# Performance work log

Measured on AMD Instinct MI355X. Metric: run time of the kernel, lower is better.

Reference implementation:

```python
import jax, jax.numpy as jnp
import numpy as np

VOCAB, INPUT, HIDDEN = 50000, 512, 1024
BATCH, MAX_LEN = 64, 256


def setup_inputs() -> dict:
    key = jax.random.key(0)
    ks = jax.random.split(key, 16)
    s = 0.02
    return {
        "last_output": jax.random.randint(ks[0], (BATCH,), 0, VOCAB),
        "last_hidden": jax.random.normal(ks[1], (BATCH, HIDDEN), jnp.float32),
        "encoder_outputs": jax.random.normal(ks[2], (MAX_LEN, BATCH, HIDDEN), jnp.float32),
        # embedding table (padding_idx=0 just means row 0 is a pad row; math is a plain gather)
        "embedding": jax.random.uniform(ks[3], (VOCAB, INPUT), jnp.float32, -0.25, 0.25),
        # concat attention: Linear(2H -> H) and v [H]
        "attn_W": jax.random.normal(ks[4], (HIDDEN, 2 * HIDDEN), jnp.float32) * s,
        "attn_b": jnp.zeros((HIDDEN,), jnp.float32),
        "v": jax.random.normal(ks[5], (HIDDEN,), jnp.float32) * s,
        # GRU (single layer): input size = INPUT + HIDDEN, gate order r,z,n (torch order)
        "W_ih": jax.random.normal(ks[6], (3 * HIDDEN, INPUT + HIDDEN), jnp.float32) * s,
        "W_hh": jax.random.uniform(ks[7], (3 * HIDDEN, HIDDEN), jnp.float32, -0.01, 0.01),
        "b_ih": jnp.zeros((3 * HIDDEN,), jnp.float32),
        "b_hh": jnp.zeros((3 * HIDDEN,), jnp.float32),
        # output projection Linear(2H -> vocab)
        "out_W": jax.random.normal(ks[8], (VOCAB, 2 * HIDDEN), jnp.float32) * s,
        "out_b": jnp.zeros((VOCAB,), jnp.float32),
    }


def reference(last_output, last_hidden, encoder_outputs, embedding,
              attn_W, attn_b, v, W_ih, W_hh, b_ih, b_hh, out_W, out_b):
    T, B, H = encoder_outputs.shape
    # --- embedding lookup: [B, INPUT]
    emb = embedding[last_output]

    # --- concat (Bahdanau-style, no tanh in original) attention, vectorized over T
    hid = jnp.broadcast_to(last_hidden[None], (T, B, H))
    cat = jnp.concatenate([hid, encoder_outputs], axis=-1)          # [T,B,2H]
    energy = jnp.einsum('tbk,hk->tbh', cat, attn_W) + attn_b        # [T,B,H]
    scores = jnp.einsum('tbh,h->bt', energy, v)                     # [B,T]
    attn = jax.nn.softmax(scores, axis=1)                           # [B,T]

    # --- context: [B,H]
    context = jnp.einsum('bt,tbh->bh', attn, encoder_outputs)

    # --- single GRU step (torch gate order r,z,n)
    x = jnp.concatenate([emb, context], axis=-1)                    # [B, INPUT+H]
    gi = x @ W_ih.T + b_ih                                          # [B,3H]
    gh = last_hidden @ W_hh.T + b_hh                                # [B,3H]
    i_r, i_z, i_n = jnp.split(gi, 3, axis=-1)
    h_r, h_z, h_n = jnp.split(gh, 3, axis=-1)
    r = jax.nn.sigmoid(i_r + h_r)
    z = jax.nn.sigmoid(i_z + h_z)
    n = jnp.tanh(i_n + r * h_n)
    h_new = (1.0 - z) * n + z * last_hidden                         # [B,H]

    # --- output projection + log_softmax over vocab
    logits = jnp.concatenate([h_new, context], axis=-1) @ out_W.T + out_b
    logp = jax.nn.log_softmax(logits, axis=-1)                      # [B,VOCAB]
    return logp, h_new
```

## Files before the change

kernel.cpp:

```cpp
#include <hip/hip_runtime.h>
#include <cstddef>

#define VOCAB  50000
#define INPUT  512
#define HIDDEN 1024
#define BATCH  64
#define MAXLEN 256
#define NBLK   625

typedef float  f32x4 __attribute__((ext_vector_type(4)));
typedef __bf16 bf16x8 __attribute__((ext_vector_type(8)));

__device__ __forceinline__ bf16x8 cvt8(float4 a, float4 b) {
    bf16x8 r;
    r[0] = (__bf16)a.x; r[1] = (__bf16)a.y; r[2] = (__bf16)a.z; r[3] = (__bf16)a.w;
    r[4] = (__bf16)b.x; r[5] = (__bf16)b.y; r[6] = (__bf16)b.z; r[7] = (__bf16)b.w;
    return r;
}

__global__ void k_u2_part(const float* __restrict__ attn_W, const float* __restrict__ v,
                          float* __restrict__ u2p) {
    int bid = blockIdx.x, tid = threadIdx.x;
    int hq = bid >> 4, kc = bid & 15;
    int kl = tid & 63, hg = tid >> 6;
    int k = kc * 64 + kl;
    float acc = 0.f;
    int h0 = hq * 256 + hg * 64;
#pragma unroll 8
    for (int h = h0; h < h0 + 64; ++h)
        acc += v[h] * attn_W[(size_t)h * (2 * HIDDEN) + HIDDEN + k];
    __shared__ float red[4][64];
    red[hg][kl] = acc;
    __syncthreads();
    if (tid < 64)
        u2p[hq * 1024 + kc * 64 + tid] =
            red[0][tid] + red[1][tid] + red[2][tid] + red[3][tid];
}

__global__ __launch_bounds__(256) void k_att(const float* __restrict__ enc,
                                             const float* __restrict__ u2p,
                                             float* __restrict__ mpart,
                                             float* __restrict__ lpart,
                                             float* __restrict__ ctxp) {
    int bid = blockIdx.x, tid = threadIdx.x;
    int b = bid >> 2, tq = bid & 3, t0 = tq * 64;
    __shared__ float u2s[1024];
    __shared__ float s_lds[64];
    __shared__ float p_lds[64];
    for (int i = tid; i < 1024; i += 256)
        u2s[i] = u2p[i] + u2p[1024 + i] + u2p[2048 + i] + u2p[3072 + i];
    __syncthreads();
    int w = tid >> 6, lane = tid & 63;
#pragma unroll 2
    for (int it = 0; it < 16; ++it) {
        int t = t0 + w * 16 + it;
        const float* row = enc + ((size_t)t * BATCH + b) * HIDDEN;
        float acc = 0.f;
#pragma unroll
        for (int i = 0; i < 4; ++i) {
            float4 e = *(const float4*)(row + lane * 4 + i * 256);
            float4 u = *(const float4*)(&u2s[lane * 4 + i * 256]);
            acc += e.x * u.x + e.y * u.y + e.z * u.z + e.w * u.w;
        }
#pragma unroll
        for (int off = 32; off; off >>= 1) acc += __shfl_down(acc, off, 64);
        if (lane == 0) s_lds[w * 16 + it] = acc;
    }
    __syncthreads();
    float m = -INFINITY;
#pragma unroll 8
    for (int t = 0; t < 64; ++t) m = fmaxf(m, s_lds[t]);
    if (tid < 64) p_lds[tid] = expf(s_lds[tid] - m);
    __syncthreads();
    float l = 0.f;
#pragma unroll 8
    for (int t = 0; t < 64; ++t) l += p_lds[t];
    float4 acc = {0.f, 0.f, 0.f, 0.f};
    const float* ebase = enc + ((size_t)t0 * BATCH + b) * HIDDEN + tid * 4;
#pragma unroll 4
    for (int t = 0; t < 64; ++t) {
        float p = p_lds[t];
        float4 e = *(const float4*)(ebase + (size_t)t * (BATCH * HIDDEN));
        acc.x += p * e.x; acc.y += p * e.y; acc.z += p * e.z; acc.w += p * e.w;
    }
    int o = b * 4 + tq;
    *(float4*)(ctxp + (size_t)o * 1024 + tid * 4) = acc;
    if (tid == 0) { mpart[o] = m; lpart[o] = l; }
}

__global__ void k_att_comb(const float* __restrict__ mpart, const float* __restrict__ lpart,
                           const float* __restrict__ ctxp,
                           const int* __restrict__ last_output,
                           const float* __restrict__ embedding,
                           const float* __restrict__ hid,
                           __bf16* __restrict__ x_bf, __bf16* __restrict__ hid_bf,
                           __bf16* __restrict__ y_bf) {
    int b = blockIdx.x >> 2, hc = blockIdx.x & 3, tid = threadIdx.x;
    float m0 = mpart[b * 4 + 0], m1 = mpart[b * 4 + 1];
    float m2 = mpart[b * 4 + 2], m3 = mpart[b * 4 + 3];
    float M = fmaxf(fmaxf(m0, m1), fmaxf(m2, m3));
    float w0 = expf(m0 - M), w1 = expf(m1 - M), w2 = expf(m2 - M), w3 = expf(m3 - M);
    float denom = lpart[b * 4 + 0] * w0 + lpart[b * 4 + 1] * w1 +
                  lpart[b * 4 + 2] * w2 + lpart[b * 4 + 3] * w3;
    float inv = 1.f / denom;
    int h = hc * 256 + tid;
    const float* cp = ctxp + (size_t)b * 4096 + h;
    float c = (w0 * cp[0] + w1 * cp[1024] + w2 * cp[2048] + w3 * cp[3072]) * inv;
    x_bf[b * 1536 + INPUT + h]  = (__bf16)c;
    y_bf[b * 2048 + HIDDEN + h] = (__bf16)c;
    if (hc < 2)
        x_bf[b * 1536 + hc * 256 + tid] =
            (__bf16)embedding[(size_t)last_output[b] * INPUT + hc * 256 + tid];
    hid_bf[b * HIDDEN + hc * 256 + tid] = (__bf16)hid[b * HIDDEN + hc * 256 + tid];
}

__device__ __forceinline__ void gemm_tile(const float* __restrict__ W,
                                          const float* __restrict__ bias,
                                          const __bf16* __restrict__ A,
                                          float* __restrict__ out,
                                          int N, int K, int jt, int tid) {
    int wid = tid >> 6, lane = tid & 63;
    int j  = jt * 16 + (lane & 15);
    int kg = (lane >> 4) * 8;
    int kchunk = K >> 2;
    int kbeg = wid * kchunk, kend = kbeg + kchunk;
    const float*  wrow = W + (size_t)j * K;
    const __bf16* arow = A + (size_t)(lane & 15) * K;
    f32x4 acc[4] = {};
    for (int k0 = kbeg; k0 < kend; k0 += 32) {
        int kk = k0 + kg;
        float4 w0 = *(const float4*)(wrow + kk);
        float4 w1 = *(const float4*)(wrow + kk + 4);
        bf16x8 bw = cvt8(w0, w1);
#pragma unroll
        for (int mt = 0; mt < 4; ++mt) {
            bf16x8 av = *(const bf16x8*)(arow + (size_t)mt * 16 * K + kk);
            acc[mt] = __builtin_amdgcn_mfma_f32_16x16x32_bf16(av, bw, acc[mt], 0, 0, 0);
        }
    }
    __shared__ float lds[4][1024];
#pragma unroll
    for (int mt = 0; mt < 4; ++mt)
#pragma unroll
        for (int r = 0; r < 4; ++r) {
            int m = mt * 16 + (lane >> 4) * 4 + r;
            lds[wid][m * 16 + (lane & 15)] = acc[mt][r];
        }
    __syncthreads();
#pragma unroll
    for (int o = tid; o < 1024; o += 256) {
        float s = lds[0][o] + lds[1][o] + lds[2][o] + lds[3][o];
        int m = o >> 4, jl = o & 15;
        out[(size_t)m * N + jt * 16 + jl] = s + bias[jt * 16 + jl];
    }
}

__global__ __launch_bounds__(256) void k_gemm_gru(const float* __restrict__ W_ih,
                                                  const float* __restrict__ b_ih,
                                                  const __bf16* __restrict__ x_bf,
                                                  float* __restrict__ Gi,
                                                  const float* __restrict__ W_hh,
                                                  const float* __restrict__ b_hh,
                                                  const __bf16* __restrict__ hid_bf,
                                                  float* __restrict__ Gh) {
    int bid = blockIdx.x, tid = threadIdx.x;
    if (bid < 192) gemm_tile(W_ih, b_ih, x_bf,  Gi, 3072, 1536, bid,       tid);
    else           gemm_tile(W_hh, b_hh, hid_bf, Gh, 3072, 1024, bid - 192, tid);
}

__global__ void k_combine(const float* __restrict__ Gi, const float* __restrict__ Gh,
                          const float* __restrict__ hid, float* __restrict__ hnew_out,
                          __bf16* __restrict__ y_bf) {
    int idx = blockIdx.x * 256 + threadIdx.x;
    int b = idx >> 10, h = idx & 1023;
    const float* gi = Gi + (size_t)b * 3072;
    const float* gh = Gh + (size_t)b * 3072;
    float r  = 1.f / (1.f + expf(-(gi[h] + gh[h])));
    float z  = 1.f / (1.f + expf(-(gi[1024 + h] + gh[1024 + h])));
    float n  = tanhf(gi[2048 + h] + r * gh[2048 + h]);
    float hp = hid[b * HIDDEN + h];
    float hn = (1.f - z) * n + z * hp;
    hnew_out[b * HIDDEN + h] = hn;
    y_bf[b * 2048 + h] = (__bf16)hn;
}

__global__ __launch_bounds__(256) void k_gemv(const float* __restrict__ W,
                                              const float* __restrict__ bias,
                                              const __bf16* __restrict__ A,
                                              float* __restrict__ out,
                                              float* __restrict__ mw,
                                              float* __restrict__ sw) {
    int bid = blockIdx.x, tid = threadIdx.x;
    int wid = tid >> 6, lane = tid & 63;
    int kg = (lane >> 4) * 8;
    int kbeg = wid * 512;
    int j0 = bid * 80 + (lane & 15);
    const float* wrow0 = W + (size_t)(j0     ) * 2048;
    const float* wrow1 = W + (size_t)(j0 + 16) * 2048;
    const float* wrow2 = W + (size_t)(j0 + 32) * 2048;
    const float* wrow3 = W + (size_t)(j0 + 48) * 2048;
    const float* wrow4 = W + (size_t)(j0 + 64) * 2048;
    const __bf16* arow = A + (size_t)(lane & 15) * 2048;
    f32x4 acc[5][4] = {};
    for (int k0 = kbeg; k0 < kbeg + 512; k0 += 32) {
        int kk = k0 + kg;
        bf16x8 bw0 = cvt8(*(const float4*)(wrow0 + kk), *(const float4*)(wrow0 + kk + 4));
        bf16x8 bw1 = cvt8(*(const float4*)(wrow1 + kk), *(const float4*)(wrow1 + kk + 4));
        bf16x8 bw2 = cvt8(*(const float4*)(wrow2 + kk), *(const float4*)(wrow2 + kk + 4));
        bf16x8 bw3 = cvt8(*(const float4*)(wrow3 + kk), *(const float4*)(wrow3 + kk + 4));
        bf16x8 bw4 = cvt8(*(const float4*)(wrow4 + kk), *(const float4*)(wrow4 + kk + 4));
#pragma unroll
        for (int mt = 0; mt < 4; ++mt) {
            bf16x8 av = *(const bf16x8*)(arow + (size_t)mt * 16 * 2048 + kk);
            acc[0][mt] = __builtin_amdgcn_mfma_f32_16x16x32_bf16(av, bw0, acc[0][mt], 0, 0, 0);
            acc[1][mt] = __builtin_amdgcn_mfma_f32_16x16x32_bf16(av, bw1, acc[1][mt], 0, 0, 0);
            acc[2][mt] = __builtin_amdgcn_mfma_f32_16x16x32_bf16(av, bw2, acc[2][mt], 0, 0, 0);
            acc[3][mt] = __builtin_amdgcn_mfma_f32_16x16x32_bf16(av, bw3, acc[3][mt], 0, 0, 0);
            acc[4][mt] = __builtin_amdgcn_mfma_f32_16x16x32_bf16(av, bw4, acc[4][mt], 0, 0, 0);
        }
    }
    __shared__ float lds[4][1024];
    float Mreg = -INFINITY, Sreg = 0.f;
#pragma unroll
    for (int u = 0; u < 5; ++u) {
        if (u) __syncthreads();
#pragma unroll
        for (int mt = 0; mt < 4; ++mt)
#pragma unroll
            for (int r = 0; r < 4; ++r) {
                int m = mt * 16 + (lane >> 4) * 4 + r;
                lds[wid][m * 16 + (lane & 15)] = acc[u][mt][r];
            }
        __syncthreads();
#pragma unroll
        for (int o = tid; o < 1024; o += 256) {
            float s = lds[0][o] + lds[1][o] + lds[2][o] + lds[3][o];
            int m = o >> 4, jl = o & 15;
            int jj = bid * 80 + u * 16 + jl;
            s += bias[jj];
            out[(size_t)m * VOCAB + jj] = s;
            lds[0][o] = s;
        }
        __syncthreads();
        if (tid < 64) {
            float mx = -INFINITY;
#pragma unroll
            for (int jl = 0; jl < 16; ++jl) mx = fmaxf(mx, lds[0][tid * 16 + jl]);
            float se = 0.f;
#pragma unroll
            for (int jl = 0; jl < 16; ++jl) se += expf(lds[0][tid * 16 + jl] - mx);
            float M2 = fmaxf(Mreg, mx);
            Sreg = Sreg * expf(Mreg - M2) + se * expf(mx - M2);
            Mreg = M2;
        }
    }
    if (tid < 64) {
        mw[(size_t)tid * NBLK + bid] = Mreg;
        sw[(size_t)tid * NBLK + bid] = Sreg;
    }
}

__global__ __launch_bounds__(256) void k_lse_fused(float* __restrict__ logits,
                                                   const float* __restrict__ mw,
                                                   const float* __restrict__ sw) {
    int bid = blockIdx.x, tid = threadIdx.x;
    int b = bid / 13, c = bid % 13;
    const float* mrow = mw + (size_t)b * NBLK;
    const float* srow = sw + (size_t)b * NBLK;
    __shared__ float red[256];
    float m = -INFINITY;
    for (int i = tid; i < NBLK; i += 256) m = fmaxf(m, mrow[i]);
    red[tid] = m; __syncthreads();
    for (int off = 128; off; off >>= 1) { if (tid < off) red[tid] = fmaxf(red[tid], red[tid + off]); __syncthreads(); }
    m = red[0]; __syncthreads();
    float s = 0.f;
    for (int i = tid; i < NBLK; i += 256) s += srow[i] * expf(mrow[i] - m);
    red[tid] = s; __syncthreads();
    for (int off = 128; off; off >>= 1) { if (tid < off) red[tid] += red[tid + off]; __syncthreads(); }
    float lse = m + logf(red[0]);
    int base = c * 4096;
    int len  = min(4096, VOCAB - base);
    float* row = logits + (size_t)b * VOCAB + base;
    for (int i = tid * 4; i < len; i += 1024) {
        float4 x = *(float4*)(row + i);
        x.x -= lse; x.y -= lse; x.z -= lse; x.w -= lse;
        *(float4*)(row + i) = x;
    }
}

extern "C" void kernel_launch(void* const* d_in, const int* in_sizes, int n_in,
                              void* d_out, int out_size, void* d_ws, size_t ws_size,
                              hipStream_t stream) {
    const int*   last_output = (const int*)  d_in[0];
    const float* last_hidden = (const float*)d_in[1];
    const float* enc         = (const float*)d_in[2];
    const float* embedding   = (const float*)d_in[3];
    const float* attn_W      = (const float*)d_in[4];
    const float* v           = (const float*)d_in[6];
    const float* W_ih        = (const float*)d_in[7];
    const float* W_hh        = (const float*)d_in[8];
    const float* b_ih        = (const float*)d_in[9];
    const float* b_hh        = (const float*)d_in[10];
    const float* out_W       = (const float*)d_in[11];
    const float* out_b       = (const float*)d_in[12];

    float* out_logp = (float*)d_out;
    float* out_hnew = (float*)d_out + (size_t)BATCH * VOCAB;

    char* ws = (char*)d_ws;
    float*  u2p     = (float*) (ws + 0);
    float*  mpart   = (float*) (ws + 16384);
    float*  lpart   = (float*) (ws + 17408);
    float*  ctxp    = (float*) (ws + 18432);
    __bf16* x_bf    = (__bf16*)(ws + 1067008);
    __bf16* hid_bf  = (__bf16*)(ws + 1263616);
    __bf16* y_bf    = (__bf16*)(ws + 1394688);
    float*  Gi      = (float*) (ws + 1656832);
    float*  Gh      = (float*) (ws + 2443264);
    float*  mw      = (float*) (ws + 3229696);
    float*  sw      = (float*) (ws + 3389696);

    k_u2_part  <<<64,   256, 0, stream>>>(attn_W, v, u2p);
    k_att      <<<256,  256, 0, stream>>>(enc, u2p, mpart, lpart, ctxp);
    k_att_comb <<<256,  256, 0, stream>>>(mpart, lpart, ctxp, last_output, embedding,
                                          last_hidden, x_bf, hid_bf, y_bf);
    k_gemm_gru <<<384,  256, 0, stream>>>(W_ih, b_ih, x_bf, Gi, W_hh, b_hh, hid_bf, Gh);
    k_combine  <<<256,  256, 0, stream>>>(Gi, Gh, last_hidden, out_hnew, y_bf);
    k_gemv     <<<NBLK, 256, 0, stream>>>(out_W, out_b, y_bf, out_logp, mw, sw);
    k_lse_fused<<<832,  256, 0, stream>>>(out_logp, mw, sw);
}
```

Before: 187.1 us.

## Fuse attention score and context passes with online softmax via LDS row staging

The attention kernel used to read each encoder row twice from global memory, once for scores and once for the weighted context sum. It now stages four rows at a time in LDS, computes their scores, and folds them into the context accumulator with an online-softmax rescale. This halves global reads of encoder_outputs, the largest input. The cost is two block barriers per 4-row step, serialized per-step dependencies, and extra expf calls per thread.

```diff
diff --git a/kernel.cpp b/kernel.cpp
--- a/kernel.cpp
+++ b/kernel.cpp
@@ -45,46 +45,50 @@
     int bid = blockIdx.x, tid = threadIdx.x;
     int b = bid >> 2, tq = bid & 3, t0 = tq * 64;
     __shared__ float u2s[1024];
-    __shared__ float s_lds[64];
-    __shared__ float p_lds[64];
+    __shared__ float erow[4][1024];
+    __shared__ float sc[4];
     for (int i = tid; i < 1024; i += 256)
         u2s[i] = u2p[i] + u2p[1024 + i] + u2p[2048 + i] + u2p[3072 + i];
     __syncthreads();
     int w = tid >> 6, lane = tid & 63;
-#pragma unroll 2
-    for (int it = 0; it < 16; ++it) {
-        int t = t0 + w * 16 + it;
+    float m = -INFINITY, l = 0.f;
+    float4 acc = {0.f, 0.f, 0.f, 0.f};
+    int h4 = tid * 4;
+    for (int r = 0; r < 16; ++r) {
+        int t = t0 + r * 4 + w;
         const float* row = enc + ((size_t)t * BATCH + b) * HIDDEN;
-        float acc = 0.f;
+        float partial = 0.f;
 #pragma unroll
         for (int i = 0; i < 4; ++i) {
-            float4 e = *(const float4*)(row + lane * 4 + i * 256);
-            float4 u = *(const float4*)(&u2s[lane * 4 + i * 256]);
-            acc += e.x * u.x + e.y * u.y + e.z * u.z + e.w * u.w;
-        }
-#pragma unroll
-        for (int off = 32; off; off >>= 1) acc += __shfl_down(acc, off, 64);
-        if (lane == 0) s_lds[w * 16 + it] = acc;
-    }
-    __syncthreads();
-    float m = -INFINITY;
-#pragma unroll 8
-    for (int t = 0; t < 64; ++t) m = fmaxf(m, s_lds[t]);
-    if (tid < 64) p_lds[tid] = expf(s_lds[tid] - m);
-    __syncthreads();
-    float l = 0.f;
-#pragma unroll 8
-    for (int t = 0; t < 64; ++t) l += p_lds[t];
-    float4 acc = {0.f, 0.f, 0.f, 0.f};
-    const float* ebase = enc + ((size_t)t0 * BATCH + b) * HIDDEN + tid * 4;
-#pragma unroll 4
-    for (int t = 0; t < 64; ++t) {
-        float p = p_lds[t];
-        float4 e = *(const float4*)(ebase + (size_t)t * (BATCH * HIDDEN));
-        acc.x += p * e.x; acc.y += p * e.y; acc.z += p * e.z; acc.w += p * e.w;
+            int h = lane * 4 + i * 256;
+            float4 e = *(const float4*)(row + h);
+            *(float4*)(&erow[w][h]) = e;
+            float4 u = *(const float4*)(&u2s[h]);
+            partial += e.x * u.x + e.y * u.y + e.z * u.z + e.w * u.w;
+        }
+#pragma unroll
+        for (int off = 32; off; off >>= 1) partial += __shfl_down(partial, off, 64);
+        if (lane == 0) sc[w] = partial;
+        __syncthreads();
+        float s0 = sc[0], s1 = sc[1], s2 = sc[2], s3 = sc[3];
+#pragma unroll
+        for (int q = 0; q < 4; ++q) {
+            float s = (q == 0) ? s0 : (q == 1) ? s1 : (q == 2) ? s2 : s3;
+            float mn = fmaxf(m, s);
+            float corr = expf(m - mn);
+            float p = expf(s - mn);
+            float4 e = *(const float4*)(&erow[q][h4]);
+            acc.x = acc.x * corr + p * e.x;
+            acc.y = acc.y * corr + p * e.y;
+            acc.z = acc.z * corr + p * e.z;
+            acc.w = acc.w * corr + p * e.w;
+            l = l * corr + p;
+            m = mn;
+        }
+        __syncthreads();
     }
     int o = b * 4 + tq;
-    *(float4*)(ctxp + (size_t)o * 1024 + tid * 4) = acc;
+    *(float4*)(ctxp + (size_t)o * 1024 + h4) = acc;
     if (tid == 0) { mpart[o] = m; lpart[o] = l; }
 }
 
```

Result: faster. 183.1 us (-2.1%).
